# Kernel optimization log

Hardware: AMD Instinct MI355X
Metric: run time of the kernel (lower is better)

The kernel has to match this reference:

```python
import jax, jax.numpy as jnp
import numpy as np

_CNOT = np.array([[1,0,0,0],[0,1,0,0],[0,0,0,1],[0,0,1,0]], dtype=np.complex64)


def _ry(t):
    c = jnp.cos(0.5 * t).astype(jnp.complex64)
    s = jnp.sin(0.5 * t).astype(jnp.complex64)
    return jnp.stack([jnp.stack([c, -s]), jnp.stack([s, c])])


def _rx(t):
    c = jnp.cos(0.5 * t).astype(jnp.complex64)
    s = (-1j * jnp.sin(0.5 * t)).astype(jnp.complex64)
    return jnp.stack([jnp.stack([c, s]), jnp.stack([s, c])])


def _rz(t):
    z = jnp.zeros((), jnp.complex64)
    em = jnp.exp(-0.5j * t).astype(jnp.complex64)
    ep = jnp.exp(0.5j * t).astype(jnp.complex64)
    return jnp.stack([jnp.stack([em, z]), jnp.stack([z, ep])])


def _apply_1q(state, gate, wire):
    # state: [B, P, 2, 2, 2, 2]; wire axis is 2 + wire
    state = jnp.moveaxis(state, 2 + wire, -1)
    state = jnp.einsum('ij,...j->...i', gate, state)
    return jnp.moveaxis(state, -1, 2 + wire)


def _apply_2q(state, gate, w1, w2):
    state = jnp.moveaxis(state, (2 + w1, 2 + w2), (-2, -1))
    sh = state.shape
    state = state.reshape(sh[:-2] + (4,))
    state = jnp.einsum('ij,...j->...i', gate, state)
    return jnp.moveaxis(state.reshape(sh), (-2, -1), (2 + w1, 2 + w2))


def _forward(x, theta, W, b):
    B = x.shape[0]
    # non-overlapping 2x2 patches, order [x[r,c], x[r,c+1], x[r+1,c], x[r+1,c+1]]
    p = x.reshape(B, 14, 2, 14, 2).transpose(0, 1, 3, 2, 4).reshape(B, 196, 4)
    half = 0.5 * p
    amp = jnp.stack([jnp.cos(half), jnp.sin(half)], axis=-1).astype(jnp.complex64)  # [B,196,4,2]
    # RY encoding from |0000> gives a product state over the 4 wires
    state = jnp.einsum('bpi,bpj,bpk,bpl->bpijkl', amp[:, :, 0], amp[:, :, 1], amp[:, :, 2], amp[:, :, 3])
    cnot = jnp.asarray(_CNOT)
    # fixed 8-op "random layer" (RandomLayer(n_ops=8) realization, 6 trainable angles)
    state = _apply_1q(state, _rx(theta[0]), 0)
    state = _apply_1q(state, _ry(theta[1]), 1)
    state = _apply_1q(state, _rz(theta[2]), 2)
    state = _apply_1q(state, _rx(theta[3]), 3)
    state = _apply_2q(state, cnot, 0, 1)
    state = _apply_2q(state, cnot, 2, 3)
    state = _apply_1q(state, _ry(theta[4]), 0)
    state = _apply_1q(state, _rz(theta[5]), 3)
    probs = state.real ** 2 + state.imag ** 2  # [B,196,2,2,2,2]
    z = jnp.array([1.0, -1.0], jnp.float32)
    e0 = jnp.einsum('bpijkl,i->bp', probs, z)
    e1 = jnp.einsum('bpijkl,j->bp', probs, z)
    e2 = jnp.einsum('bpijkl,k->bp', probs, z)
    e3 = jnp.einsum('bpijkl,l->bp', probs, z)
    feats = jnp.stack([e0, e1, e2, e3], axis=-1).reshape(B, 4 * 14 * 14)
    logits = feats @ W.T + b
    return jax.nn.log_softmax(logits, axis=-1)


def setup_inputs() -> dict:
    key = jax.random.key(0)
    k1, k2, k3 = jax.random.split(key, 3)
    B = 4096
    x = jax.random.uniform(k1, (B, 28, 28), dtype=jnp.float32) * np.float32(np.pi)
    theta = jax.random.uniform(k2, (6,), dtype=jnp.float32) * np.float32(2 * np.pi)
    W = jax.random.normal(k3, (10, 784), dtype=jnp.float32) * 0.02
    b = jnp.zeros((10,), jnp.float32)
    return {"x": x, "theta": theta, "W": W, "b": b}


def reference(x, theta, W, b):
    return _forward(x, theta, W, b)
```

## Files before the change

### kernel.cpp

```cpp
#include <hip/hip_runtime.h>
#include <math.h>


typedef __attribute__((ext_vector_type(2))) _Float16 half2v;

static __device__ __forceinline__ float fdot2f(half2v a, half2v b, float c) {
#if __has_builtin(__builtin_amdgcn_fdot2)
    return __builtin_amdgcn_fdot2(a, b, c, false);
#else
    return c + (float)a.x * (float)b.x + (float)a.y * (float)b.y;
#endif
}

static __device__ __forceinline__ unsigned int pkh2(float a, float b) {
#if __has_builtin(__builtin_amdgcn_cvt_pkrtz)
    return __builtin_bit_cast(unsigned int, __builtin_amdgcn_cvt_pkrtz(a, b));
#else
    half2v h = { (_Float16)a, (_Float16)b };
    return __builtin_bit_cast(unsigned int, h);
#endif
}

static __device__ __forceinline__ half2v ash2(unsigned int u) {
    return __builtin_bit_cast(half2v, u);
}

__global__ __launch_bounds__(256) void quanv_fused_kernel(
    const float* __restrict__ x,
    const float* __restrict__ theta,
    const float* __restrict__ W,
    const float* __restrict__ bias,
    float* __restrict__ out)
{
    __shared__ uint4 Wlds[980];

    const int tid  = threadIdx.x;
    const int wave = tid >> 6;
    const int lane = tid & 63;
    const int b    = blockIdx.x * 4 + wave;

    {
        const float4* __restrict__ Wg = reinterpret_cast<const float4*>(W);
        for (int g = tid; g < 980; g += 256) {
            const int p  = g % 196;
            const int kk = g / 196;
            const float4 fa = Wg[(2 * kk)     * 196 + p];
            const float4 fb = Wg[(2 * kk + 1) * 196 + p];
            Wlds[p * 5 + kk] = make_uint4(pkh2(fa.x, fa.y), pkh2(fa.z, fa.w),
                                          pkh2(fb.x, fb.y), pkh2(fb.z, fb.w));
        }
    }
    __syncthreads();

    const float t1 = theta[1];
    const float K1 = __cosf(theta[0]) * __cosf(theta[4]);
    const float K2 = __sinf(theta[4]);
    const float K3 = __cosf(theta[0]);
    const float K4 = __cosf(theta[3]);

    const float* __restrict__ xb = x + (size_t)b * 784;

    float acc[10];
#pragma unroll
    for (int k = 0; k < 10; ++k) acc[k] = 0.f;

    auto do_patch = [&](int p) {
        const int r = p / 14, c = p - r * 14;
        const float* px = xb + r * 56 + c * 2;
        const float2 t01 = *reinterpret_cast<const float2*>(px);
        const float2 t23 = *reinterpret_cast<const float2*>(px + 28);

        float sp0, cp0, sph, cph;
        __sincosf(t01.x, &sp0, &cp0);
        __sincosf(t01.y + t1, &sph, &cph);
        const float cp2 = __cosf(t23.x);
        const float cp3 = __cosf(t23.y);

        const float e0 = K1 * cp0 - K2 * sp0 * sph;
        const float e1 = K3 * cp0 * cph;
        const float e2 = cp2;
        const float e3 = K4 * cp2 * cp3;

        const half2v e01 = ash2(pkh2(e0, e1));
        const half2v e23 = ash2(pkh2(e2, e3));

        const uint4* __restrict__ row = &Wlds[p * 5];
#pragma unroll
        for (int kk = 0; kk < 5; ++kk) {
            const uint4 w = row[kk];
            acc[2 * kk]     = fdot2f(ash2(w.x), e01, acc[2 * kk]);
            acc[2 * kk]     = fdot2f(ash2(w.y), e23, acc[2 * kk]);
            acc[2 * kk + 1] = fdot2f(ash2(w.z), e01, acc[2 * kk + 1]);
            acc[2 * kk + 1] = fdot2f(ash2(w.w), e23, acc[2 * kk + 1]);
        }
    };

#pragma unroll
    for (int i = 0; i < 3; ++i) do_patch(lane + 64 * i);
    if (lane < 4) do_patch(192 + lane);

#pragma unroll
    for (int m = 1; m < 64; m <<= 1) {
#pragma unroll
        for (int k = 0; k < 10; ++k) acc[k] += __shfl_xor(acc[k], m, 64);
    }

    float v = acc[0];
#pragma unroll
    for (int k = 1; k < 10; ++k) v = (lane == k) ? acc[k] : v;
    v += bias[lane < 10 ? lane : 0];

    float m = (lane < 10) ? v : -1e30f;
#pragma unroll
    for (int off = 1; off < 16; off <<= 1) m = fmaxf(m, __shfl_xor(m, off, 16));
    float s = (lane < 10) ? __expf(v - m) : 0.f;
#pragma unroll
    for (int off = 1; off < 16; off <<= 1) s += __shfl_xor(s, off, 16);
    const float lse = m + __logf(s);

    if (lane < 10) out[(size_t)b * 10 + lane] = v - lse;
}

extern "C" void kernel_launch(void* const* d_in, const int* in_sizes, int n_in,
                              void* d_out, int out_size, void* d_ws, size_t ws_size,
                              hipStream_t stream) {
    const float* x     = (const float*)d_in[0];
    const float* theta = (const float*)d_in[1];
    const float* W     = (const float*)d_in[2];
    const float* bias  = (const float*)d_in[3];
    float* out = (float*)d_out;

    const int B = in_sizes[0] / 784;
    quanv_fused_kernel<<<dim3(B / 4), dim3(256), 0, stream>>>(x, theta, W, bias, out);
}
```

Baseline: 11.59 us.

## Process two batch rows per wave to reuse LDS weight loads

Each wave now handles two samples instead of one, so every W row read from LDS feeds dot products for both samples. The grid is halved, which also halves the per-block work of staging and converting W into LDS. The softmax stage packs both samples into 16-lane groups of one wave. This costs more registers for the second accumulator set and leaves fewer blocks to hide latency.

Result: faster. 11.25 us (-3.0%).

```diff
diff --git a/kernel.cpp b/kernel.cpp
--- a/kernel.cpp
+++ b/kernel.cpp
@@ -35,9 +35,9 @@
     __shared__ uint4 Wlds[980];
 
     const int tid  = threadIdx.x;
-    const int wave = tid >> 6;
+    const int wv   = tid >> 6;
     const int lane = tid & 63;
-    const int b    = blockIdx.x * 4 + wave;
+    const int b0   = blockIdx.x * 8 + wv * 2;
 
     {
         const float4* __restrict__ Wg = reinterpret_cast<const float4*>(W);
@@ -58,40 +58,50 @@
     const float K3 = __cosf(theta[0]);
     const float K4 = __cosf(theta[3]);
 
-    const float* __restrict__ xb = x + (size_t)b * 784;
+    const float* __restrict__ xa = x + (size_t)b0 * 784;
+    const float* __restrict__ xb = xa + 784;
 
-    float acc[10];
+    float acc0[10], acc1[10];
 #pragma unroll
-    for (int k = 0; k < 10; ++k) acc[k] = 0.f;
+    for (int k = 0; k < 10; ++k) { acc0[k] = 0.f; acc1[k] = 0.f; }
 
-    auto do_patch = [&](int p) {
-        const int r = p / 14, c = p - r * 14;
-        const float* px = xb + r * 56 + c * 2;
-        const float2 t01 = *reinterpret_cast<const float2*>(px);
-        const float2 t23 = *reinterpret_cast<const float2*>(px + 28);
-
+    auto evec = [&](const float* __restrict__ xs, const float* px_off,
+                    unsigned int& e01, unsigned int& e23, int off) {
+        const float2 t01 = *reinterpret_cast<const float2*>(px_off + off);
+        const float2 t23 = *reinterpret_cast<const float2*>(px_off + off + 28);
         float sp0, cp0, sph, cph;
         __sincosf(t01.x, &sp0, &cp0);
         __sincosf(t01.y + t1, &sph, &cph);
         const float cp2 = __cosf(t23.x);
         const float cp3 = __cosf(t23.y);
-
         const float e0 = K1 * cp0 - K2 * sp0 * sph;
         const float e1 = K3 * cp0 * cph;
-        const float e2 = cp2;
-        const float e3 = K4 * cp2 * cp3;
+        e01 = pkh2(e0, e1);
+        e23 = pkh2(cp2, K4 * cp2 * cp3);
+        (void)xs;
+    };
 
-        const half2v e01 = ash2(pkh2(e0, e1));
-        const half2v e23 = ash2(pkh2(e2, e3));
+    auto do_patch = [&](int p) {
+        const int r = p / 14, c = p - r * 14;
+        const int off = r * 56 + c * 2;
+        unsigned int a01, a23, b01, b23;
+        evec(xa, xa, a01, a23, off);
+        evec(xb, xb, b01, b23, off);
+        const half2v ea01 = ash2(a01), ea23 = ash2(a23);
+        const half2v eb01 = ash2(b01), eb23 = ash2(b23);
 
         const uint4* __restrict__ row = &Wlds[p * 5];
 #pragma unroll
         for (int kk = 0; kk < 5; ++kk) {
             const uint4 w = row[kk];
-            acc[2 * kk]     = fdot2f(ash2(w.x), e01, acc[2 * kk]);
-            acc[2 * kk]     = fdot2f(ash2(w.y), e23, acc[2 * kk]);
-            acc[2 * kk + 1] = fdot2f(ash2(w.z), e01, acc[2 * kk + 1]);
-            acc[2 * kk + 1] = fdot2f(ash2(w.w), e23, acc[2 * kk + 1]);
+            acc0[2 * kk]     = fdot2f(ash2(w.x), ea01, acc0[2 * kk]);
+            acc0[2 * kk]     = fdot2f(ash2(w.y), ea23, acc0[2 * kk]);
+            acc0[2 * kk + 1] = fdot2f(ash2(w.z), ea01, acc0[2 * kk + 1]);
+            acc0[2 * kk + 1] = fdot2f(ash2(w.w), ea23, acc0[2 * kk + 1]);
+            acc1[2 * kk]     = fdot2f(ash2(w.x), eb01, acc1[2 * kk]);
+            acc1[2 * kk]     = fdot2f(ash2(w.y), eb23, acc1[2 * kk]);
+            acc1[2 * kk + 1] = fdot2f(ash2(w.z), eb01, acc1[2 * kk + 1]);
+            acc1[2 * kk + 1] = fdot2f(ash2(w.w), eb23, acc1[2 * kk + 1]);
         }
     };
 
@@ -102,23 +112,31 @@
 #pragma unroll
     for (int m = 1; m < 64; m <<= 1) {
 #pragma unroll
-        for (int k = 0; k < 10; ++k) acc[k] += __shfl_xor(acc[k], m, 64);
+        for (int k = 0; k < 10; ++k) {
+            acc0[k] += __shfl_xor(acc0[k], m, 64);
+            acc1[k] += __shfl_xor(acc1[k], m, 64);
+        }
     }
 
-    float v = acc[0];
+    float v = acc0[0];
 #pragma unroll
-    for (int k = 1; k < 10; ++k) v = (lane == k) ? acc[k] : v;
-    v += bias[lane < 10 ? lane : 0];
+    for (int k = 1; k < 10; ++k) v = (lane == k) ? acc0[k] : v;
+#pragma unroll
+    for (int k = 0; k < 10; ++k) v = (lane == 16 + k) ? acc1[k] : v;
 
-    float m = (lane < 10) ? v : -1e30f;
+    const int cls = lane & 15;
+    const bool act = (cls < 10) && (lane < 32);
+    v += bias[cls < 10 ? cls : 0];
+
+    float m = act ? v : -1e30f;
 #pragma unroll
     for (int off = 1; off < 16; off <<= 1) m = fmaxf(m, __shfl_xor(m, off, 16));
-    float s = (lane < 10) ? __expf(v - m) : 0.f;
+    float s = act ? __expf(v - m) : 0.f;
 #pragma unroll
     for (int off = 1; off < 16; off <<= 1) s += __shfl_xor(s, off, 16);
     const float lse = m + __logf(s);
 
-    if (lane < 10) out[(size_t)b * 10 + lane] = v - lse;
+    if (act) out[(size_t)(b0 + (lane >> 4)) * 10 + cls] = v - lse;
 }
 
 extern "C" void kernel_launch(void* const* d_in, const int* in_sizes, int n_in,
@@ -131,5 +149,5 @@
     float* out = (float*)d_out;
 
     const int B = in_sizes[0] / 784;
-    quanv_fused_kernel<<<dim3(B / 4), dim3(256), 0, stream>>>(x, theta, W, bias, out);
+    quanv_fused_kernel<<<dim3(B / 8), dim3(256), 0, stream>>>(x, theta, W, bias, out);
 }
```
